# Performance work log

Hardware: AMD Instinct MI355X
Metric: run time of the kernel (lower is better)

The kernel has to match this reference:

```python
import jax, jax.numpy as jnp
import numpy as np

NUM_CLASSES = 5
OVERLAP = 0.5
THRESH = 0.3


def _decode(loc, defaults):
    # loc: [N,2] (center offset, log-width offset); defaults: [N,2] (center, width)
    c = defaults[:, 0] + loc[:, 0] * defaults[:, 1]
    w = defaults[:, 1] * jnp.exp(loc[:, 1])
    return jnp.stack([c - 0.5 * w, c + 0.5 * w], axis=1)  # [N,2] start/end


def _nms_keep(boxes, scores, valid, overlap):
    # boxes [N,2], scores [N], valid [N] bool -> keep mask [N] bool (original order)
    N = scores.shape[0]
    masked = jnp.where(valid, scores, -jnp.inf)
    order = jnp.argsort(-masked)               # descending by score
    b = boxes[order]
    v = valid[order]
    start, end = b[:, 0], b[:, 1]
    length = end - start
    inter = jnp.clip(jnp.minimum(end[:, None], end[None, :]) -
                     jnp.maximum(start[:, None], start[None, :]), 0.0)
    union = length[:, None] + length[None, :] - inter
    iou = inter / jnp.maximum(union, 1e-12)
    idx = jnp.arange(N)
    # suppress_mat[i,j]: j is lower-ranked than i and overlaps i above threshold
    suppress_mat = (iou > overlap) & (idx[None, :] > idx[:, None])

    def body(i, keep):
        sup = keep[i] & suppress_mat[i]
        return keep & ~sup

    keep_sorted = jax.lax.fori_loop(0, N, body, v)
    return jnp.zeros((N,), bool).at[order].set(keep_sorted)


def setup_inputs() -> dict:
    key = jax.random.key(0)
    k1, k2, k3, k4 = jax.random.split(key, 4)
    B, N, C = 8, 2048, NUM_CLASSES
    localizations = 0.5 * jax.random.normal(k1, (B, N, 2), dtype=jnp.float32)
    classifications = 2.0 * jax.random.normal(k2, (B, N, C), dtype=jnp.float32)
    centers = jax.random.uniform(k3, (N, 1), dtype=jnp.float32)               # in [0,1]
    widths = 0.01 + 0.05 * jax.random.uniform(k4, (N, 1), dtype=jnp.float32)  # positive
    localizations_default = jnp.concatenate([centers, widths], axis=1)
    return {"localizations": localizations,
            "classifications": classifications,
            "localizations_default": localizations_default}


def reference(localizations, classifications, localizations_default):
    # softmax over classes
    scores = jax.nn.softmax(classifications, axis=2)             # [B,N,C]
    decoded = jax.vmap(_decode, in_axes=(0, None))(localizations, localizations_default)  # [B,N,2]
    cls_scores = jnp.transpose(scores[:, :, 1:], (0, 2, 1))      # [B,C-1,N] (skip background)
    valid = cls_scores > THRESH                                  # per-class threshold filter

    nms_per_class = jax.vmap(lambda s, v, bx: _nms_keep(bx, s, v, OVERLAP),
                             in_axes=(0, 0, None))               # over classes
    keep = jax.vmap(nms_per_class, in_axes=(0, 0, 0))(cls_scores, valid, decoded)  # [B,C-1,N]

    # final sanity filter: start > -10 and end < 10
    in_range = (decoded[:, :, 0] > -10.0) & (decoded[:, :, 1] < 10.0)  # [B,N]
    keep = keep & in_range[:, None, :]

    # dense output: (start, end, score) per kept event, zeros elsewhere -> [B,C-1,N,3]
    boxes_bc = jnp.broadcast_to(decoded[:, None, :, :], keep.shape + (2,))
    out = jnp.concatenate([boxes_bc, cls_scores[..., None]], axis=-1)
    return out * keep[..., None].astype(out.dtype)
```

## Files before the change

kernel.cpp:

```cpp
#include <hip/hip_runtime.h>
#include <math.h>

#define N_ANCHORS 2048
#define THRESH 0.3f
#define OVERLAP 0.5f
#define NBC 32
#define BLOCK 1024
#define NW 16
#define BUCKET_BASE 32051


__global__ __launch_bounds__(BLOCK, 1) void det_mono(
    const float* __restrict__ loc, const float* __restrict__ cls,
    const float* __restrict__ defs, float* __restrict__ out)
{
#pragma clang fp contract(off)
    const int tid  = threadIdx.x;
    const int lane = tid & 63;
    const int wid  = tid >> 6;
    const int bc   = blockIdx.x;
    const int b    = bc >> 2;
    const int c    = bc & 3;

    __shared__ __align__(16) float          csc[2048];
    __shared__ __align__(16) float2         cbx[2048];
    __shared__                unsigned short cid[2048];
    __shared__ __align__(16) float2         sbox[2048];
    __shared__                float          ssc[2048];
    __shared__                unsigned short sid[2048];
    __shared__ __align__(16) float4         kbx[2048];
    __shared__                unsigned short blist[2048];
    __shared__ int s_hist[512];
    __shared__ int s_off[512];
    __shared__ unsigned long long diag[64];
    __shared__ unsigned long long deadp[NW];
    __shared__ unsigned long long keptg[32];
    __shared__ int s_wsum[NW], s_woff[NW], s_V, s_K;

    float* const outb = out + (size_t)bc * N_ANCHORS * 3;
    {
        float4 z4 = make_float4(0.f, 0.f, 0.f, 0.f);
        float4* ob4 = (float4*)outb;
#pragma unroll 1
        for (int i = tid; i < (N_ANCHORS * 3) / 4; i += BLOCK) ob4[i] = z4;
    }
    if (tid < 32) keptg[tid] = 0ull;
    if (tid < 512) s_hist[tid] = 0;
    if (tid == 0) s_K = 0;

    const int base = tid * 2;
    float c10[10], l4v[4], d4v[4];
    {
        const float2* cp2 = (const float2*)(cls + ((size_t)b * N_ANCHORS + base) * 5);
#pragma unroll
        for (int q = 0; q < 5; ++q) ((float2*)c10)[q] = cp2[q];
        ((float4*)l4v)[0] = *(const float4*)(loc + ((size_t)b * N_ANCHORS + base) * 2);
        ((float4*)d4v)[0] = *(const float4*)(defs + (size_t)base * 2);
    }
    float sc2[2], bs2[2], be2[2];
    int vmask = 0;
#pragma unroll
    for (int k = 0; k < 2; ++k) {
        float x0 = c10[5*k+0], x1 = c10[5*k+1], x2 = c10[5*k+2],
              x3 = c10[5*k+3], x4 = c10[5*k+4];
        float m  = fmaxf(fmaxf(fmaxf(fmaxf(x0, x1), x2), x3), x4);
        float e0 = expf(x0 - m), e1 = expf(x1 - m), e2 = expf(x2 - m),
              e3 = expf(x3 - m), e4 = expf(x4 - m);
        float sum = e0 + e1 + e2 + e3 + e4;
        float ec  = (c == 0) ? e1 : (c == 1) ? e2 : (c == 2) ? e3 : e4;
        float score = ec / sum;
        float l0 = l4v[2*k], l1 = l4v[2*k+1];
        float d0 = d4v[2*k], d1 = d4v[2*k+1];
        float cc = d0 + l0 * d1;
        float w  = d1 * expf(l1);
        sc2[k] = score;
        bs2[k] = cc - 0.5f * w;
        be2[k] = cc + 0.5f * w;
        if (score > THRESH) vmask |= (1 << k);
    }

    const unsigned long long lmlt = (1ull << lane) - 1ull;
    unsigned long long b0 = __ballot(vmask & 1);
    unsigned long long b1 = __ballot(vmask & 2);
    int exc  = __popcll(b0 & lmlt) + __popcll(b1 & lmlt);
    if (lane == 0) s_wsum[wid] = __popcll(b0) + __popcll(b1);
    __syncthreads();
    if (tid == 0) {
        int o = 0;
        for (int w = 0; w < NW; ++w) { s_woff[w] = o; o += s_wsum[w]; }
        s_V = o;
    }
    __syncthreads();
    {
        int off = s_woff[wid] + exc;
#pragma unroll
        for (int k = 0; k < 2; ++k) {
            if (vmask & (1 << k)) {
                csc[off] = sc2[k];
                cbx[off] = make_float2(bs2[k], be2[k]);
                cid[off] = (unsigned short)(base + k);
                off++;
            }
        }
    }
    __syncthreads();
    const int V = s_V;
    const int W = (V + 63) >> 6;
    const int SCend = W << 6;

#pragma unroll 1
    for (int p = tid; p < V; p += BLOCK) {
        unsigned bkt = (__float_as_uint(csc[p]) >> 15) - BUCKET_BASE;
        atomicAdd(&s_hist[bkt], 1);
    }
    __syncthreads();
    if (wid == 0) {
        int running = 0;
#pragma unroll 1
        for (int ch = 0; ch < 8; ++ch) {
            int bidx = 511 - ((ch << 6) + lane);
            int v = s_hist[bidx];
            int incv = v;
#pragma unroll
            for (int d = 1; d < 64; d <<= 1) {
                int t = __shfl_up(incv, d);
                if (lane >= d) incv += t;
            }
            s_off[bidx] = running + incv - v;
            running += __shfl(incv, 63);
        }
    }
    __syncthreads();
#pragma unroll 1
    for (int p = tid; p < V; p += BLOCK) {
        unsigned bkt = (__float_as_uint(csc[p]) >> 15) - BUCKET_BASE;
        int slot = atomicAdd(&s_off[bkt], 1);
        blist[slot] = (unsigned short)p;
    }
    __syncthreads();
#pragma unroll 1
    for (int p = tid; p < V; p += BLOCK) {
        float s = csc[p];
        unsigned bkt = (__float_as_uint(s) >> 15) - BUCKET_BASE;
        int end = s_off[bkt], cnt = s_hist[bkt];
        int r = end - cnt;
#pragma unroll 1
        for (int t = end - cnt; t < end; ++t) {
            int e = blist[t];
            float s2 = csc[e];
            r += (s2 > s || (s2 == s && e < p)) ? 1 : 0;
        }
        sbox[r] = cbx[p];
        ssc[r]  = s;
        sid[r]  = cid[p];
    }
#pragma unroll 1
    for (int i = V + tid; i < SCend; i += BLOCK)
        sbox[i] = make_float2(1e30f, 1e30f);
    __syncthreads();

#pragma unroll 1
    for (int g = 0; g < W; ++g) {
        const int u = (g << 6) + lane;
        const float2 cb = sbox[u];
        const float  cl = cb.y - cb.x;

        const int K = s_K;
        bool dead = false;
#pragma unroll 1
        for (int i = wid; i < K; i += NW) {
            float4 kb = kbx[i];
            float in = fmaxf(fminf(cb.y, kb.y) - fmaxf(cb.x, kb.x), 0.0f);
            float un = kb.z + cl - in;
            dead |= (in > OVERLAP * fmaxf(un, 1e-12f));
        }
        {
            unsigned long long db = __ballot(dead);
            if (lane == 0) deadp[wid] = db;
        }

#pragma unroll
        for (int q = 0; q < 4; ++q) {
            const int r = (wid << 2) + q;
            const float2 rb = sbox[(g << 6) + r];
            const float  rl = rb.y - rb.x;
            float in = fmaxf(fminf(rb.y, cb.y) - fmaxf(rb.x, cb.x), 0.0f);
            float un = cl + rl - in;
            bool sup = (in > OVERLAP * fmaxf(un, 1e-12f));
            unsigned long long bal = __ballot(sup);
            if (lane == 0) diag[r] = bal & ((1ull << r) - 1ull);
        }
        __syncthreads();

        if (wid == 0) {
            unsigned long long dw = 0ull;
#pragma unroll
            for (int i = 0; i < NW; ++i) dw |= deadp[i];
            const unsigned long long rself = diag[lane];
            int rem = V - (g << 6);
            unsigned long long valid = (rem >= 64) ? ~0ull : ((1ull << rem) - 1ull);
            unsigned long long cand = valid & ~dw;
            unsigned long long kw = 0ull;
            while (cand) {
                unsigned long long suppw = __ballot((rself & cand) != 0ull);
                unsigned long long nk = cand & ~suppw;
                if (!nk) nk = cand & (~cand + 1ull);
                kw |= nk;
                unsigned long long ddw = __ballot((rself & nk) != 0ull);
                cand &= ~(nk | ddw);
            }
            if ((kw >> lane) & 1ull) {
                int pos = s_K + __popcll(kw & ((1ull << lane) - 1ull));
                kbx[pos] = make_float4(cb.x, cb.y, cl, 0.f);
            }
            if (lane == 0) { keptg[g] = kw; s_K += __popcll(kw); }
        }
        __syncthreads();
    }

#pragma unroll 1
    for (int r = tid; r < V; r += BLOCK) {
        if ((keptg[r >> 6] >> (r & 63)) & 1ull) {
            float2 bx = sbox[r];
            if (bx.x > -10.0f && bx.y < 10.0f) {
                int n = sid[r];
                float* o = outb + (size_t)n * 3;
                o[0] = bx.x;
                o[1] = bx.y;
                o[2] = ssc[r];
            }
        }
    }
}

extern "C" void kernel_launch(void* const* d_in, const int* in_sizes, int n_in,
                              void* d_out, int out_size, void* d_ws, size_t ws_size,
                              hipStream_t stream) {
    const float* loc  = (const float*)d_in[0];
    const float* cls  = (const float*)d_in[1];
    const float* defs = (const float*)d_in[2];
    float* out = (float*)d_out;
    (void)d_ws; (void)ws_size;
    det_mono<<<NBC, BLOCK, 0, stream>>>(loc, cls, defs, out);
}
```

Measured before the change: 77.87 us.

## Precompute triangular block suppression bitmask matrix for small candidate counts

```diff
diff --git a/kernel.cpp b/kernel.cpp
--- a/kernel.cpp
+++ b/kernel.cpp
@@ -8,6 +8,7 @@
 #define BLOCK 1024
 #define NW 16
 #define BUCKET_BASE 32051
+#define WMAX 12
 
 
 __global__ __launch_bounds__(BLOCK, 1) void det_mono(
@@ -32,9 +33,11 @@
     __shared__                unsigned short blist[2048];
     __shared__ int s_hist[512];
     __shared__ int s_off[512];
+    __shared__ __align__(16) unsigned long long mat[78 * 64];
     __shared__ unsigned long long diag[64];
     __shared__ unsigned long long deadp[NW];
     __shared__ unsigned long long keptg[32];
+    __shared__ unsigned long long s_kv[WMAX];
     __shared__ int s_wsum[NW], s_woff[NW], s_V, s_K;
 
     float* const outb = out + (size_t)bc * N_ANCHORS * 3;
@@ -159,63 +162,117 @@
         sbox[i] = make_float2(1e30f, 1e30f);
     __syncthreads();
 
-#pragma unroll 1
-    for (int g = 0; g < W; ++g) {
-        const int u = (g << 6) + lane;
-        const float2 cb = sbox[u];
-        const float  cl = cb.y - cb.x;
-
-        const int K = s_K;
-        bool dead = false;
-#pragma unroll 1
-        for (int i = wid; i < K; i += NW) {
-            float4 kb = kbx[i];
-            float in = fmaxf(fminf(cb.y, kb.y) - fmaxf(cb.x, kb.x), 0.0f);
-            float un = kb.z + cl - in;
-            dead |= (in > OVERLAP * fmaxf(un, 1e-12f));
-        }
+    if (W <= WMAX) {
+        const int TRIW = (W * (W + 1)) >> 1;
         {
-            unsigned long long db = __ballot(dead);
-            if (lane == 0) deadp[wid] = db;
-        }
-
-#pragma unroll
-        for (int q = 0; q < 4; ++q) {
-            const int r = (wid << 2) + q;
-            const float2 rb = sbox[(g << 6) + r];
-            const float  rl = rb.y - rb.x;
-            float in = fmaxf(fminf(rb.y, cb.y) - fmaxf(rb.x, cb.x), 0.0f);
-            float un = cl + rl - in;
-            bool sup = (in > OVERLAP * fmaxf(un, 1e-12f));
-            unsigned long long bal = __ballot(sup);
-            if (lane == 0) diag[r] = bal & ((1ull << r) - 1ull);
+            int k = 0, w = wid;
+            while (w > k) { w -= (k + 1); ++k; }
+#pragma unroll 1
+            for (int t = wid; t < TRIW; t += NW) {
+                const float2 myb = sbox[(w << 6) + lane];
+                const float  myl = myb.y - myb.x;
+                unsigned long long myword = 0ull;
+#pragma unroll 1
+                for (int r = 0; r < 64; ++r) {
+                    const float2 vb = sbox[(k << 6) + r];
+                    const float  vl = vb.y - vb.x;
+                    float in = fmaxf(fminf(vb.y, myb.y) - fmaxf(vb.x, myb.x), 0.0f);
+                    float un = myl + vl - in;
+                    bool sup = (in > OVERLAP * fmaxf(un, 1e-12f));
+                    unsigned long long bal = __ballot(sup);
+                    if (w == k) bal &= (1ull << r) - 1ull;
+                    myword = (lane == r) ? bal : myword;
+                }
+                mat[((size_t)t << 6) + lane] = myword;
+                w += NW;
+                while (w > k) { w -= (k + 1); ++k; }
+            }
         }
         __syncthreads();
 
         if (wid == 0) {
-            unsigned long long dw = 0ull;
-#pragma unroll
-            for (int i = 0; i < NW; ++i) dw |= deadp[i];
-            const unsigned long long rself = diag[lane];
-            int rem = V - (g << 6);
-            unsigned long long valid = (rem >= 64) ? ~0ull : ((1ull << rem) - 1ull);
-            unsigned long long cand = valid & ~dw;
-            unsigned long long kw = 0ull;
-            while (cand) {
-                unsigned long long suppw = __ballot((rself & cand) != 0ull);
-                unsigned long long nk = cand & ~suppw;
-                if (!nk) nk = cand & (~cand + 1ull);
-                kw |= nk;
-                unsigned long long ddw = __ballot((rself & nk) != 0ull);
-                cand &= ~(nk | ddw);
-            }
-            if ((kw >> lane) & 1ull) {
-                int pos = s_K + __popcll(kw & ((1ull << lane) - 1ull));
-                kbx[pos] = make_float4(cb.x, cb.y, cl, 0.f);
-            }
-            if (lane == 0) { keptg[g] = kw; s_K += __popcll(kw); }
+#pragma unroll 1
+            for (int g = 0; g < W; ++g) {
+                const int gbase = (g * (g + 1)) >> 1;
+                unsigned long long dl_or = 0ull;
+#pragma unroll 1
+                for (int w2 = 0; w2 < g; ++w2)
+                    dl_or |= mat[((size_t)(gbase + w2) << 6) + lane] & s_kv[w2];
+                const unsigned long long rself = mat[((size_t)(gbase + g) << 6) + lane];
+                int rem = V - (g << 6);
+                unsigned long long valid = (rem >= 64) ? ~0ull : ((1ull << rem) - 1ull);
+                unsigned long long cand = valid & ~__ballot(dl_or != 0ull);
+                unsigned long long kw = 0ull;
+                while (cand) {
+                    unsigned long long suppw = __ballot((rself & cand) != 0ull);
+                    unsigned long long nk = cand & ~suppw;
+                    if (!nk) nk = cand & (~cand + 1ull);
+                    kw |= nk;
+                    unsigned long long ddw = __ballot((rself & nk) != 0ull);
+                    cand &= ~(nk | ddw);
+                }
+                if (lane == 0) { s_kv[g] = kw; keptg[g] = kw; }
+            }
         }
         __syncthreads();
+    } else {
+#pragma unroll 1
+        for (int g = 0; g < W; ++g) {
+            const int u = (g << 6) + lane;
+            const float2 cb = sbox[u];
+            const float  cl = cb.y - cb.x;
+
+            const int K = s_K;
+            bool dead = false;
+#pragma unroll 1
+            for (int i = wid; i < K; i += NW) {
+                float4 kb = kbx[i];
+                float in = fmaxf(fminf(cb.y, kb.y) - fmaxf(cb.x, kb.x), 0.0f);
+                float un = kb.z + cl - in;
+                dead |= (in > OVERLAP * fmaxf(un, 1e-12f));
+            }
+            {
+                unsigned long long db = __ballot(dead);
+                if (lane == 0) deadp[wid] = db;
+            }
+#pragma unroll
+            for (int q = 0; q < 4; ++q) {
+                const int r = (wid << 2) + q;
+                const float2 rb = sbox[(g << 6) + r];
+                const float  rl = rb.y - rb.x;
+                float in = fmaxf(fminf(rb.y, cb.y) - fmaxf(rb.x, cb.x), 0.0f);
+                float un = cl + rl - in;
+                bool sup = (in > OVERLAP * fmaxf(un, 1e-12f));
+                unsigned long long bal = __ballot(sup);
+                if (lane == 0) diag[r] = bal & ((1ull << r) - 1ull);
+            }
+            __syncthreads();
+
+            if (wid == 0) {
+                unsigned long long dw = 0ull;
+#pragma unroll
+                for (int i = 0; i < NW; ++i) dw |= deadp[i];
+                const unsigned long long rself = diag[lane];
+                int rem = V - (g << 6);
+                unsigned long long valid = (rem >= 64) ? ~0ull : ((1ull << rem) - 1ull);
+                unsigned long long cand = valid & ~dw;
+                unsigned long long kw = 0ull;
+                while (cand) {
+                    unsigned long long suppw = __ballot((rself & cand) != 0ull);
+                    unsigned long long nk = cand & ~suppw;
+                    if (!nk) nk = cand & (~cand + 1ull);
+                    kw |= nk;
+                    unsigned long long ddw = __ballot((rself & nk) != 0ull);
+                    cand &= ~(nk | ddw);
+                }
+                if ((kw >> lane) & 1ull) {
+                    int pos = s_K + __popcll(kw & ((1ull << lane) - 1ull));
+                    kbx[pos] = make_float4(cb.x, cb.y, cl, 0.f);
+                }
+                if (lane == 0) { keptg[g] = kw; s_K += __popcll(kw); }
+            }
+            __syncthreads();
+        }
     }
 
 #pragma unroll 1
```

New measurement: 89.81 us. 1.15x slower.
